# Kernel tuning notes

Hardware: AMD Instinct MI355X
Metric: run time of the kernel (lower is better)

Reference implementation:

```python
import jax, jax.numpy as jnp
import numpy as np
import math

N_HEAD = 16
N_FEAT = 1024
O_FEAT = 1024
D_K = N_FEAT // N_HEAD


def setup_inputs() -> dict:
    key = jax.random.key(0)
    ks = jax.random.split(key, 11)
    B, L, DIN = 4, 2048, 1024
    s_in = 1.0 / math.sqrt(DIN)
    s_f = 1.0 / math.sqrt(N_FEAT)
    return {
        "query": jax.random.normal(ks[0], (B, L, DIN), jnp.float32),
        "key": jax.random.normal(ks[1], (B, L, DIN), jnp.float32),
        "value": jax.random.normal(ks[2], (B, L, DIN), jnp.float32),
        "Wq": jax.random.uniform(ks[3], (DIN, N_FEAT), jnp.float32, -s_in, s_in),
        "bq": jax.random.uniform(ks[4], (N_FEAT,), jnp.float32, -s_in, s_in),
        "Wk": jax.random.uniform(ks[5], (DIN, N_FEAT), jnp.float32, -s_in, s_in),
        "bk": jax.random.uniform(ks[6], (N_FEAT,), jnp.float32, -s_in, s_in),
        "Wv": jax.random.uniform(ks[7], (DIN, N_FEAT), jnp.float32, -s_in, s_in),
        "bv": jax.random.uniform(ks[8], (N_FEAT,), jnp.float32, -s_in, s_in),
        "Wo": jax.random.uniform(ks[9], (N_FEAT, O_FEAT), jnp.float32, -s_f, s_f),
        "bo": jax.random.uniform(ks[10], (O_FEAT,), jnp.float32, -s_f, s_f),
    }


def reference(query, key, value, Wq, bq, Wk, bk, Wv, bv, Wo, bo):
    B = query.shape[0]
    # QKV projections -> [B, H, L, Dk]
    def proj(x, W, b):
        y = x @ W + b
        return y.reshape(B, -1, N_HEAD, D_K).transpose(0, 2, 1, 3)
    q = proj(query, Wq, bq)
    k = proj(key, Wk, bk)
    v = proj(value, Wv, bv)
    # naive attention: full [B,H,Lq,Lk] scores
    scores = jnp.einsum("bhqd,bhkd->bhqk", q, k) / math.sqrt(D_K)
    attn = jax.nn.softmax(scores, axis=-1)  # dropout_rate=0 -> identity
    x = jnp.einsum("bhqk,bhkd->bhqd", attn, v)
    x = x.transpose(0, 2, 1, 3).reshape(B, -1, N_FEAT)
    return x @ Wo + bo
```

## Files before the change

### kernel.cpp

```cpp
#include <hip/hip_runtime.h>
#include <hip/hip_bf16.h>

#define DM 1024
#define LQ 2048

typedef __attribute__((ext_vector_type(8))) short short8;
typedef __attribute__((ext_vector_type(4))) float floatx4;

#define MFMA16(a, b, c) __builtin_amdgcn_mfma_f32_16x16x32_bf16((a), (b), (c), 0, 0, 0)

__device__ __forceinline__ unsigned short f2b(float f) {
  union { float f; unsigned u; } x; x.f = f;
  unsigned u = x.u;
  unsigned r = (u + 0x7fffu + ((u >> 16) & 1u)) >> 16;
  return (unsigned short)r;
}

__device__ __forceinline__ unsigned cvt_pk(float lo, float hi) {
  unsigned r;
  asm("v_cvt_pk_bf16_f32 %0, %1, %2" : "=v"(r) : "v"(lo), "v"(hi));
  return r;
}
__device__ __forceinline__ uint4 pack16(float4 a, float4 b) {
  return make_uint4(cvt_pk(a.x, a.y), cvt_pk(a.z, a.w),
                    cvt_pk(b.x, b.y), cvt_pk(b.z, b.w));
}

__device__ __forceinline__ void gl_lds16(const void* g, void* l) {
  __builtin_amdgcn_global_load_lds(
      (const __attribute__((address_space(1))) void*)g,
      (__attribute__((address_space(3))) void*)l, 16, 0, 0);
}

__device__ __forceinline__ void xcd_tiles(int bx, int by, int* m0, int* n0) {
  int flat = bx + (by << 3);
  int xcd = flat & 7;
  int loc = flat >> 3;
  *m0 = (xcd * 8 + (loc >> 3)) * 128;
  *n0 = (loc & 7) * 128;
}

__global__ __launch_bounds__(256) void transpose_w4(
    const float* __restrict__ W0, const float* __restrict__ W1,
    const float* __restrict__ W2, const float* __restrict__ W3,
    unsigned short* __restrict__ T0, unsigned short* __restrict__ T1,
    unsigned short* __restrict__ T2, unsigned short* __restrict__ T3) {
  __shared__ unsigned short t[64][65];
  const float* src; unsigned short* dst;
  switch (blockIdx.z) {
    case 0: src = W0; dst = T0; break;
    case 1: src = W1; dst = T1; break;
    case 2: src = W2; dst = T2; break;
    default: src = W3; dst = T3; break;
  }
  const int x = threadIdx.x & 63;
  const int y4 = threadIdx.x >> 6;
  const int c0 = blockIdx.x * 64;
  const int r0 = blockIdx.y * 64;
#pragma unroll
  for (int i = 0; i < 16; ++i) {
    int r = y4 * 16 + i;
    t[r][x] = f2b(src[(size_t)(r0 + r) * 1024 + c0 + x]);
  }
  __syncthreads();
#pragma unroll
  for (int i = 0; i < 16; ++i) {
    int r = y4 * 16 + i;
    dst[(size_t)(c0 + r) * 1024 + r0 + x] = t[x][r];
  }
}

__global__ __launch_bounds__(256) void gemm_qkv(
    const float* __restrict__ Aq, const float* __restrict__ Ak,
    const float* __restrict__ Av,
    const unsigned short* __restrict__ BtQ, const unsigned short* __restrict__ BtK,
    const unsigned short* __restrict__ BtV,
    const float* __restrict__ bq, const float* __restrict__ bk,
    const float* __restrict__ bv,
    unsigned short* __restrict__ Qb, unsigned short* __restrict__ Kb,
    unsigned short* __restrict__ Vt) {
  const int K = 1024, N = 1024;
  __shared__ unsigned short As[128 * 32];
  __shared__ unsigned short Bs[128 * 32];
  const int z = blockIdx.z;
  const float* A; const unsigned short* Bt; const float* bias;
  if (z == 0) { A = Aq; Bt = BtQ; bias = bq; }
  else if (z == 1) { A = Ak; Bt = BtK; bias = bk; }
  else { A = Av; Bt = BtV; bias = bv; }

  const int tid = threadIdx.x;
  const int wave = tid >> 6;
  const int lane = tid & 63;
  const int fm = lane & 15;
  const int quad = lane >> 4;
  int m0, n0;
  xcd_tiles(blockIdx.x, blockIdx.y, &m0, &n0);
  const int wm = (wave >> 1) * 64;
  const int wn = (wave & 1) * 64;

  floatx4 acc[4][4];
#pragma unroll
  for (int i = 0; i < 4; ++i)
#pragma unroll
    for (int j = 0; j < 4; ++j) acc[i][j] = (floatx4){0.f, 0.f, 0.f, 0.f};

  const int srow = lane >> 2;
  const int scol = (lane & 3) * 8;
  const float* Ag = A + (size_t)(m0 + wave * 32 + srow) * K + scol;
  const unsigned short* Bg = Bt + (size_t)(n0 + wave * 32 + srow) * K + scol;
  unsigned short* AsB = &As[(wave * 32) * 32];
  unsigned short* Bsl = &Bs[(wave * 32) * 32];

  for (int k0 = 0; k0 < K; k0 += 32) {
    float4 f0 = *(const float4*)(Ag + k0);
    float4 f1 = *(const float4*)(Ag + k0 + 4);
    float4 f2 = *(const float4*)(Ag + k0 + (size_t)16 * K);
    float4 f3 = *(const float4*)(Ag + k0 + (size_t)16 * K + 4);
    gl_lds16(Bg + k0, Bsl);
    gl_lds16(Bg + k0 + (size_t)16 * K, Bsl + 16 * 32);
    *(uint4*)&AsB[lane * 8] = pack16(f0, f1);
    *(uint4*)&AsB[16 * 32 + lane * 8] = pack16(f2, f3);
    __syncthreads();
    short8 a[4], b[4];
#pragma unroll
    for (int i = 0; i < 4; ++i)
      a[i] = *(const short8*)&As[(wm + i * 16 + fm) * 32 + quad * 8];
#pragma unroll
    for (int j = 0; j < 4; ++j)
      b[j] = *(const short8*)&Bs[(wn + j * 16 + fm) * 32 + quad * 8];
#pragma unroll
    for (int i = 0; i < 4; ++i)
#pragma unroll
      for (int j = 0; j < 4; ++j) acc[i][j] = MFMA16(a[i], b[j], acc[i][j]);
    __syncthreads();
  }

  float bvv[4];
#pragma unroll
  for (int j = 0; j < 4; ++j) bvv[j] = bias[n0 + wn + j * 16 + fm];

  if (z < 2) {
    const float sc = (z == 0) ? 0.1803368801111204f : 1.0f;
    unsigned short* C = (z == 0) ? Qb : Kb;
#pragma unroll
    for (int i = 0; i < 4; ++i) {
      int row = m0 + wm + i * 16 + quad * 4;
#pragma unroll
      for (int j = 0; j < 4; ++j) {
        int col = n0 + wn + j * 16 + fm;
#pragma unroll
        for (int r = 0; r < 4; ++r)
          C[(size_t)(row + r) * N + col] = f2b((acc[i][j][r] + bvv[j]) * sc);
      }
    }
  } else {
#pragma unroll
    for (int i = 0; i < 4; ++i) {
      int row = m0 + wm + i * 16 + quad * 4;
      int b = row >> 11, l = row & 2047;
#pragma unroll
      for (int j = 0; j < 4; ++j) {
        int col = n0 + wn + j * 16 + fm;
        int h = col >> 6, d = col & 63;
        uint2 pk;
        pk.x = cvt_pk(acc[i][j][0] + bvv[j], acc[i][j][1] + bvv[j]);
        pk.y = cvt_pk(acc[i][j][2] + bvv[j], acc[i][j][3] + bvv[j]);
        *(uint2*)&Vt[(((size_t)b * 16 + h) * 64 + d) * 2048 + l] = pk;
      }
    }
  }
}

__global__ __launch_bounds__(256) void gemm_bt_bias_f32(
    const unsigned short* __restrict__ A, const unsigned short* __restrict__ Bt,
    const float* __restrict__ bias, float* __restrict__ C,
    int M, int N, int K) {
  __shared__ unsigned short As[128 * 32];
  __shared__ unsigned short Bs[128 * 32];
  const int tid = threadIdx.x;
  const int wave = tid >> 6;
  const int lane = tid & 63;
  const int fm = lane & 15;
  const int quad = lane >> 4;
  int m0, n0;
  xcd_tiles(blockIdx.x, blockIdx.y, &m0, &n0);
  const int wm = (wave >> 1) * 64;
  const int wn = (wave & 1) * 64;

  floatx4 acc[4][4];
#pragma unroll
  for (int i = 0; i < 4; ++i)
#pragma unroll
    for (int j = 0; j < 4; ++j) acc[i][j] = (floatx4){0.f, 0.f, 0.f, 0.f};

  const int srow = lane >> 2;
  const int scol = (lane & 3) * 8;
  const unsigned short* Ag = A + (size_t)(m0 + wave * 32 + srow) * K + scol;
  const unsigned short* Bg = Bt + (size_t)(n0 + wave * 32 + srow) * K + scol;
  unsigned short* Asl = &As[(wave * 32) * 32];
  unsigned short* Bsl = &Bs[(wave * 32) * 32];

  for (int k0 = 0; k0 < K; k0 += 32) {
    gl_lds16(Ag + k0, Asl);
    gl_lds16(Ag + k0 + (size_t)16 * K, Asl + 16 * 32);
    gl_lds16(Bg + k0, Bsl);
    gl_lds16(Bg + k0 + (size_t)16 * K, Bsl + 16 * 32);
    __syncthreads();
    short8 a[4], b[4];
#pragma unroll
    for (int i = 0; i < 4; ++i)
      a[i] = *(const short8*)&As[(wm + i * 16 + fm) * 32 + quad * 8];
#pragma unroll
    for (int j = 0; j < 4; ++j)
      b[j] = *(const short8*)&Bs[(wn + j * 16 + fm) * 32 + quad * 8];
#pragma unroll
    for (int i = 0; i < 4; ++i)
#pragma unroll
      for (int j = 0; j < 4; ++j) acc[i][j] = MFMA16(a[i], b[j], acc[i][j]);
    __syncthreads();
  }

  float bv[4];
#pragma unroll
  for (int j = 0; j < 4; ++j) bv[j] = bias[n0 + wn + j * 16 + fm];
#pragma unroll
  for (int i = 0; i < 4; ++i) {
    int row = m0 + wm + i * 16 + quad * 4;
#pragma unroll
    for (int j = 0; j < 4; ++j) {
      int col = n0 + wn + j * 16 + fm;
#pragma unroll
      for (int r = 0; r < 4; ++r)
        C[(size_t)(row + r) * N + col] = acc[i][j][r] + bv[j];
    }
  }
}

__global__ __launch_bounds__(256, 4) void attn_kernel(
    const unsigned short* Qb, const unsigned short* __restrict__ Kb,
    const unsigned short* __restrict__ Vtg, unsigned short* Xb) {
  __shared__ unsigned short Ks[64 * 72];
  __shared__ unsigned short Vts[64 * 72];
  __shared__ unsigned short Ps[4 * 32 * 72];
  unsigned short* Qs = Ps;

  const int tid = threadIdx.x;
  const int wave = tid >> 6;
  const int lane = tid & 63;
  const int fm = lane & 15;
  const int quad = lane >> 4;
  const int qt = blockIdx.x;
  const int bh = blockIdx.y;
  const size_t base = (size_t)(bh >> 4) * (LQ * DM) + (size_t)(bh & 15) * 64;
  const unsigned short* Vg = Vtg + (size_t)bh * 64 * 2048;
  const int q0 = qt * 128;

#pragma unroll
  for (int it = 0; it < 4; ++it) {
    int idx = it * 256 + tid;
    int r = idx >> 3;
    int cc = (idx & 7) * 8;
    *(short8*)&Qs[r * 72 + cc] =
        *(const short8*)(Qb + base + (size_t)(q0 + r) * DM + cc);
  }
  __syncthreads();
  short8 qf[2][2];
#pragma unroll
  for (int mt = 0; mt < 2; ++mt)
#pragma unroll
    for (int ks = 0; ks < 2; ++ks)
      qf[mt][ks] = *(const short8*)&Qs[(wave * 32 + mt * 16 + fm) * 72 + ks * 32 + quad * 8];
  __syncthreads();

  short8 ones;
#pragma unroll
  for (int i = 0; i < 8; ++i) ones[i] = (short)0x3F80;

  floatx4 lacc[2];
  lacc[0] = (floatx4){0.f, 0.f, 0.f, 0.f};
  lacc[1] = (floatx4){0.f, 0.f, 0.f, 0.f};
  floatx4 oacc[4][2];
#pragma unroll
  for (int dt = 0; dt < 4; ++dt)
#pragma unroll
    for (int mt = 0; mt < 2; ++mt) oacc[dt][mt] = (floatx4){0.f, 0.f, 0.f, 0.f};

  unsigned short* Pw = &Ps[wave * 32 * 72];

  const int srow0 = tid >> 3;
  const int scc = (tid & 7) * 8;
  short8 kr[2], vr[2];
#pragma unroll
  for (int it = 0; it < 2; ++it) {
    int row = it * 32 + srow0;
    kr[it] = *(const short8*)(Kb + base + (size_t)row * DM + scc);
    vr[it] = *(const short8*)(Vg + (size_t)row * 2048 + scc);
  }

  for (int kt = 0; kt < 32; ++kt) {
    __syncthreads();
#pragma unroll
    for (int it = 0; it < 2; ++it) {
      int row = it * 32 + srow0;
      *(short8*)&Ks[row * 72 + scc] = kr[it];
      *(short8*)&Vts[row * 72 + scc] = vr[it];
    }
    __syncthreads();
    if (kt < 31) {
      int k0n = (kt + 1) * 64;
#pragma unroll
      for (int it = 0; it < 2; ++it) {
        int row = it * 32 + srow0;
        kr[it] = *(const short8*)(Kb + base + (size_t)(k0n + row) * DM + scc);
        vr[it] = *(const short8*)(Vg + (size_t)row * 2048 + k0n + scc);
      }
    }

    floatx4 sacc[4][2];
#pragma unroll
    for (int jt = 0; jt < 4; ++jt)
#pragma unroll
      for (int mt = 0; mt < 2; ++mt) sacc[jt][mt] = (floatx4){0.f, 0.f, 0.f, 0.f};
#pragma unroll
    for (int jt = 0; jt < 4; ++jt) {
      short8 k0f = *(const short8*)&Ks[(jt * 16 + fm) * 72 + quad * 8];
      short8 k1f = *(const short8*)&Ks[(jt * 16 + fm) * 72 + 32 + quad * 8];
#pragma unroll
      for (int mt = 0; mt < 2; ++mt) {
        sacc[jt][mt] = MFMA16(k0f, qf[mt][0], sacc[jt][mt]);
        sacc[jt][mt] = MFMA16(k1f, qf[mt][1], sacc[jt][mt]);
      }
    }

#pragma unroll
    for (int mt = 0; mt < 2; ++mt) {
      int rowoff = (mt * 16 + fm) * 72;
#pragma unroll
      for (int jt = 0; jt < 4; ++jt) {
        float p0 = __builtin_amdgcn_exp2f(sacc[jt][mt][0]);
        float p1 = __builtin_amdgcn_exp2f(sacc[jt][mt][1]);
        float p2 = __builtin_amdgcn_exp2f(sacc[jt][mt][2]);
        float p3 = __builtin_amdgcn_exp2f(sacc[jt][mt][3]);
        uint2 pk;
        pk.x = cvt_pk(p0, p1);
        pk.y = cvt_pk(p2, p3);
        *(uint2*)&Pw[rowoff + jt * 16 + quad * 4] = pk;
      }
    }

    __threadfence_block();

#pragma unroll
    for (int ks = 0; ks < 2; ++ks) {
      short8 pf0 = *(const short8*)&Pw[fm * 72 + ks * 32 + quad * 8];
      short8 pf1 = *(const short8*)&Pw[(16 + fm) * 72 + ks * 32 + quad * 8];
      lacc[0] = MFMA16(ones, pf0, lacc[0]);
      lacc[1] = MFMA16(ones, pf1, lacc[1]);
#pragma unroll
      for (int dt = 0; dt < 4; ++dt) {
        short8 vf = *(const short8*)&Vts[(dt * 16 + fm) * 72 + ks * 32 + quad * 8];
        oacc[dt][0] = MFMA16(vf, pf0, oacc[dt][0]);
        oacc[dt][1] = MFMA16(vf, pf1, oacc[dt][1]);
      }
    }
  }

  float inv[2];
  inv[0] = 1.0f / lacc[0][0];
  inv[1] = 1.0f / lacc[1][0];

#pragma unroll
  for (int mt = 0; mt < 2; ++mt) {
    int q = q0 + wave * 32 + mt * 16 + fm;
#pragma unroll
    for (int dt = 0; dt < 4; ++dt) {
      uint2 o;
      o.x = cvt_pk(oacc[dt][mt][0] * inv[mt], oacc[dt][mt][1] * inv[mt]);
      o.y = cvt_pk(oacc[dt][mt][2] * inv[mt], oacc[dt][mt][3] * inv[mt]);
      *(uint2*)&Xb[base + (size_t)q * DM + dt * 16 + quad * 4] = o;
    }
  }
}

extern "C" void kernel_launch(void* const* d_in, const int* in_sizes, int n_in,
                              void* d_out, int out_size, void* d_ws, size_t ws_size,
                              hipStream_t stream) {
  const float* q_in = (const float*)d_in[0];
  const float* k_in = (const float*)d_in[1];
  const float* v_in = (const float*)d_in[2];
  const float* Wq = (const float*)d_in[3];
  const float* bq = (const float*)d_in[4];
  const float* Wk = (const float*)d_in[5];
  const float* bk = (const float*)d_in[6];
  const float* Wv = (const float*)d_in[7];
  const float* bv = (const float*)d_in[8];
  const float* Wo = (const float*)d_in[9];
  const float* bo = (const float*)d_in[10];
  float* out = (float*)d_out;

  char* w = (char*)d_ws;
  unsigned short* WqT = (unsigned short*)w; w += 1024 * 1024 * 2;
  unsigned short* WkT = (unsigned short*)w; w += 1024 * 1024 * 2;
  unsigned short* WvT = (unsigned short*)w; w += 1024 * 1024 * 2;
  unsigned short* WoT = (unsigned short*)w; w += 1024 * 1024 * 2;
  unsigned short* Qb  = (unsigned short*)w; w += (size_t)8192 * 1024 * 2;
  unsigned short* Kb  = (unsigned short*)w; w += (size_t)8192 * 1024 * 2;
  unsigned short* Vt  = (unsigned short*)w; w += (size_t)8192 * 1024 * 2;
  unsigned short* Xb  = Qb;

  transpose_w4<<<dim3(16, 16, 4), 256, 0, stream>>>(Wq, Wk, Wv, Wo,
                                                    WqT, WkT, WvT, WoT);

  gemm_qkv<<<dim3(8, 64, 3), 256, 0, stream>>>(
      q_in, k_in, v_in, WqT, WkT, WvT, bq, bk, bv, Qb, Kb, Vt);

  attn_kernel<<<dim3(16, 64), 256, 0, stream>>>(Qb, Kb, Vt, Xb);

  gemm_bt_bias_f32<<<dim3(8, 64), 256, 0, stream>>>(Xb, WoT, bo, out, 8192, 1024, 1024);
}
```

Measured before the change: 369.2 us.

## Double-buffer GEMM LDS tiles and pre-convert QKV activations to bf16

Both projection GEMMs now keep two LDS stages. The next K-tile is issued with global_load_lds while the current one is consumed, using vmcnt waits and raw barriers instead of a load, sync, compute, sync loop. The fp32 query/key/value inputs are first converted to bf16 by a separate kernel, so the QKV GEMM can stream A through direct global-to-LDS loads. This costs an extra pass over 96 MB of fp32 input plus 48 MB of bf16 writes, more workspace, and doubled LDS per block, which may reduce occupancy.

```diff
diff --git a/kernel.cpp b/kernel.cpp
--- a/kernel.cpp
+++ b/kernel.cpp
@@ -8,6 +8,10 @@
 typedef __attribute__((ext_vector_type(4))) float floatx4;
 
 #define MFMA16(a, b, c) __builtin_amdgcn_mfma_f32_16x16x32_bf16((a), (b), (c), 0, 0, 0)
+#define BAR() __builtin_amdgcn_s_barrier()
+#define FENCE() asm volatile("" ::: "memory")
+#define VWAIT4() asm volatile("s_waitcnt vmcnt(4)" ::: "memory")
+#define VWAIT0() asm volatile("s_waitcnt vmcnt(0)" ::: "memory")
 
 __device__ __forceinline__ unsigned short f2b(float f) {
   union { float f; unsigned u; } x; x.f = f;
@@ -38,6 +42,19 @@
   int loc = flat >> 3;
   *m0 = (xcd * 8 + (loc >> 3)) * 128;
   *n0 = (loc & 7) * 128;
+}
+
+__global__ __launch_bounds__(256) void cvt3(
+    const float* __restrict__ A0, const float* __restrict__ A1,
+    const float* __restrict__ A2,
+    unsigned short* __restrict__ O0, unsigned short* __restrict__ O1,
+    unsigned short* __restrict__ O2) {
+  const float* s = (blockIdx.z == 0) ? A0 : (blockIdx.z == 1) ? A1 : A2;
+  unsigned short* d = (blockIdx.z == 0) ? O0 : (blockIdx.z == 1) ? O1 : O2;
+  size_t i = ((size_t)blockIdx.x * 256 + threadIdx.x) * 8;
+  float4 f0 = *(const float4*)(s + i);
+  float4 f1 = *(const float4*)(s + i + 4);
+  *(uint4*)(d + i) = pack16(f0, f1);
 }
 
 __global__ __launch_bounds__(256) void transpose_w4(
@@ -70,9 +87,10 @@
   }
 }
 
+
 __global__ __launch_bounds__(256) void gemm_qkv(
-    const float* __restrict__ Aq, const float* __restrict__ Ak,
-    const float* __restrict__ Av,
+    const unsigned short* __restrict__ Aq, const unsigned short* __restrict__ Ak,
+    const unsigned short* __restrict__ Av,
     const unsigned short* __restrict__ BtQ, const unsigned short* __restrict__ BtK,
     const unsigned short* __restrict__ BtV,
     const float* __restrict__ bq, const float* __restrict__ bk,
@@ -80,10 +98,10 @@
     unsigned short* __restrict__ Qb, unsigned short* __restrict__ Kb,
     unsigned short* __restrict__ Vt) {
   const int K = 1024, N = 1024;
-  __shared__ unsigned short As[128 * 32];
-  __shared__ unsigned short Bs[128 * 32];
+  __shared__ unsigned short As[2][128 * 32];
+  __shared__ unsigned short Bs[2][128 * 32];
   const int z = blockIdx.z;
-  const float* A; const unsigned short* Bt; const float* bias;
+  const unsigned short* A; const unsigned short* Bt; const float* bias;
   if (z == 0) { A = Aq; Bt = BtQ; bias = bq; }
   else if (z == 1) { A = Ak; Bt = BtK; bias = bk; }
   else { A = Av; Bt = BtV; bias = bv; }
@@ -106,33 +124,60 @@
 
   const int srow = lane >> 2;
   const int scol = (lane & 3) * 8;
-  const float* Ag = A + (size_t)(m0 + wave * 32 + srow) * K + scol;
+  const unsigned short* Ag = A + (size_t)(m0 + wave * 32 + srow) * K + scol;
   const unsigned short* Bg = Bt + (size_t)(n0 + wave * 32 + srow) * K + scol;
-  unsigned short* AsB = &As[(wave * 32) * 32];
-  unsigned short* Bsl = &Bs[(wave * 32) * 32];
-
-  for (int k0 = 0; k0 < K; k0 += 32) {
-    float4 f0 = *(const float4*)(Ag + k0);
-    float4 f1 = *(const float4*)(Ag + k0 + 4);
-    float4 f2 = *(const float4*)(Ag + k0 + (size_t)16 * K);
-    float4 f3 = *(const float4*)(Ag + k0 + (size_t)16 * K + 4);
-    gl_lds16(Bg + k0, Bsl);
-    gl_lds16(Bg + k0 + (size_t)16 * K, Bsl + 16 * 32);
-    *(uint4*)&AsB[lane * 8] = pack16(f0, f1);
-    *(uint4*)&AsB[16 * 32 + lane * 8] = pack16(f2, f3);
-    __syncthreads();
+  const int stA = wave * 32 * 32;
+
+#pragma unroll
+  for (int t = 0; t < 2; ++t) {
+    gl_lds16(Ag + t * 32, &As[t][stA]);
+    gl_lds16(Ag + t * 32 + (size_t)16 * K, &As[t][stA + 16 * 32]);
+    gl_lds16(Bg + t * 32, &Bs[t][stA]);
+    gl_lds16(Bg + t * 32 + (size_t)16 * K, &Bs[t][stA + 16 * 32]);
+  }
+
+#pragma unroll 1
+  for (int t = 0; t < 30; ++t) {
+    const int buf = t & 1;
+    VWAIT4();
+    BAR();
+    FENCE();
     short8 a[4], b[4];
 #pragma unroll
     for (int i = 0; i < 4; ++i)
-      a[i] = *(const short8*)&As[(wm + i * 16 + fm) * 32 + quad * 8];
+      a[i] = *(const short8*)&As[buf][(wm + i * 16 + fm) * 32 + quad * 8];
 #pragma unroll
     for (int j = 0; j < 4; ++j)
-      b[j] = *(const short8*)&Bs[(wn + j * 16 + fm) * 32 + quad * 8];
+      b[j] = *(const short8*)&Bs[buf][(wn + j * 16 + fm) * 32 + quad * 8];
 #pragma unroll
     for (int i = 0; i < 4; ++i)
 #pragma unroll
       for (int j = 0; j < 4; ++j) acc[i][j] = MFMA16(a[i], b[j], acc[i][j]);
-    __syncthreads();
+    BAR();
+    FENCE();
+    const int tn = t + 2;
+    gl_lds16(Ag + tn * 32, &As[buf][stA]);
+    gl_lds16(Ag + tn * 32 + (size_t)16 * K, &As[buf][stA + 16 * 32]);
+    gl_lds16(Bg + tn * 32, &Bs[buf][stA]);
+    gl_lds16(Bg + tn * 32 + (size_t)16 * K, &Bs[buf][stA + 16 * 32]);
+  }
+#pragma unroll
+  for (int t = 30; t < 32; ++t) {
+    if (t == 30) VWAIT4(); else VWAIT0();
+    BAR();
+    FENCE();
+    const int buf = t & 1;
+    short8 a[4], b[4];
+#pragma unroll
+    for (int i = 0; i < 4; ++i)
+      a[i] = *(const short8*)&As[buf][(wm + i * 16 + fm) * 32 + quad * 8];
+#pragma unroll
+    for (int j = 0; j < 4; ++j)
+      b[j] = *(const short8*)&Bs[buf][(wn + j * 16 + fm) * 32 + quad * 8];
+#pragma unroll
+    for (int i = 0; i < 4; ++i)
+#pragma unroll
+      for (int j = 0; j < 4; ++j) acc[i][j] = MFMA16(a[i], b[j], acc[i][j]);
   }
 
   float bvv[4];
@@ -175,8 +220,8 @@
     const unsigned short* __restrict__ A, const unsigned short* __restrict__ Bt,
     const float* __restrict__ bias, float* __restrict__ C,
     int M, int N, int K) {
-  __shared__ unsigned short As[128 * 32];
-  __shared__ unsigned short Bs[128 * 32];
+  __shared__ unsigned short As[2][128 * 32];
+  __shared__ unsigned short Bs[2][128 * 32];
   const int tid = threadIdx.x;
   const int wave = tid >> 6;
   const int lane = tid & 63;
@@ -197,27 +242,58 @@
   const int scol = (lane & 3) * 8;
   const unsigned short* Ag = A + (size_t)(m0 + wave * 32 + srow) * K + scol;
   const unsigned short* Bg = Bt + (size_t)(n0 + wave * 32 + srow) * K + scol;
-  unsigned short* Asl = &As[(wave * 32) * 32];
-  unsigned short* Bsl = &Bs[(wave * 32) * 32];
-
-  for (int k0 = 0; k0 < K; k0 += 32) {
-    gl_lds16(Ag + k0, Asl);
-    gl_lds16(Ag + k0 + (size_t)16 * K, Asl + 16 * 32);
-    gl_lds16(Bg + k0, Bsl);
-    gl_lds16(Bg + k0 + (size_t)16 * K, Bsl + 16 * 32);
-    __syncthreads();
+  const int stA = wave * 32 * 32;
+
+#pragma unroll
+  for (int t = 0; t < 2; ++t) {
+    gl_lds16(Ag + t * 32, &As[t][stA]);
+    gl_lds16(Ag + t * 32 + (size_t)16 * K, &As[t][stA + 16 * 32]);
+    gl_lds16(Bg + t * 32, &Bs[t][stA]);
+    gl_lds16(Bg + t * 32 + (size_t)16 * K, &Bs[t][stA + 16 * 32]);
+  }
+
+#pragma unroll 1
+  for (int t = 0; t < 30; ++t) {
+    const int buf = t & 1;
+    VWAIT4();
+    BAR();
+    FENCE();
     short8 a[4], b[4];
 #pragma unroll
     for (int i = 0; i < 4; ++i)
-      a[i] = *(const short8*)&As[(wm + i * 16 + fm) * 32 + quad * 8];
+      a[i] = *(const short8*)&As[buf][(wm + i * 16 + fm) * 32 + quad * 8];
 #pragma unroll
     for (int j = 0; j < 4; ++j)
-      b[j] = *(const short8*)&Bs[(wn + j * 16 + fm) * 32 + quad * 8];
+      b[j] = *(const short8*)&Bs[buf][(wn + j * 16 + fm) * 32 + quad * 8];
 #pragma unroll
     for (int i = 0; i < 4; ++i)
 #pragma unroll
       for (int j = 0; j < 4; ++j) acc[i][j] = MFMA16(a[i], b[j], acc[i][j]);
-    __syncthreads();
+    BAR();
+    FENCE();
+    const int tn = t + 2;
+    gl_lds16(Ag + tn * 32, &As[buf][stA]);
+    gl_lds16(Ag + tn * 32 + (size_t)16 * K, &As[buf][stA + 16 * 32]);
+    gl_lds16(Bg + tn * 32, &Bs[buf][stA]);
+    gl_lds16(Bg + tn * 32 + (size_t)16 * K, &Bs[buf][stA + 16 * 32]);
+  }
+#pragma unroll
+  for (int t = 30; t < 32; ++t) {
+    if (t == 30) VWAIT4(); else VWAIT0();
+    BAR();
+    FENCE();
+    const int buf = t & 1;
+    short8 a[4], b[4];
+#pragma unroll
+    for (int i = 0; i < 4; ++i)
+      a[i] = *(const short8*)&As[buf][(wm + i * 16 + fm) * 32 + quad * 8];
+#pragma unroll
+    for (int j = 0; j < 4; ++j)
+      b[j] = *(const short8*)&Bs[buf][(wn + j * 16 + fm) * 32 + quad * 8];
+#pragma unroll
+    for (int i = 0; i < 4; ++i)
+#pragma unroll
+      for (int j = 0; j < 4; ++j) acc[i][j] = MFMA16(a[i], b[j], acc[i][j]);
   }
 
   float bv[4];
@@ -406,13 +482,18 @@
   unsigned short* Qb  = (unsigned short*)w; w += (size_t)8192 * 1024 * 2;
   unsigned short* Kb  = (unsigned short*)w; w += (size_t)8192 * 1024 * 2;
   unsigned short* Vt  = (unsigned short*)w; w += (size_t)8192 * 1024 * 2;
+  unsigned short* Qa  = (unsigned short*)w; w += (size_t)8192 * 1024 * 2;
+  unsigned short* Ka  = (unsigned short*)w; w += (size_t)8192 * 1024 * 2;
+  unsigned short* Va  = (unsigned short*)w; w += (size_t)8192 * 1024 * 2;
   unsigned short* Xb  = Qb;
 
   transpose_w4<<<dim3(16, 16, 4), 256, 0, stream>>>(Wq, Wk, Wv, Wo,
                                                     WqT, WkT, WvT, WoT);
 
+  cvt3<<<dim3(4096, 1, 3), 256, 0, stream>>>(q_in, k_in, v_in, Qa, Ka, Va);
+
   gemm_qkv<<<dim3(8, 64, 3), 256, 0, stream>>>(
-      q_in, k_in, v_in, WqT, WkT, WvT, bq, bk, bv, Qb, Kb, Vt);
+      Qa, Ka, Va, WqT, WkT, WvT, bq, bk, bv, Qb, Kb, Vt);
 
   attn_kernel<<<dim3(16, 64), 256, 0, stream>>>(Qb, Kb, Vt, Xb);
 
```

After: 352.5 us. 4.5% less time.
